# Optimization experiments

Measured on AMD Instinct MI355X. Metric: run time of the kernel, lower is better.

Reference implementation:

```python
import jax, jax.numpy as jnp
import numpy as np

EPS = 1e-12
K_APPNP = 3
ALPHA = 0.5

def setup_inputs() -> dict:
    key = jax.random.key(0)
    kg, kz, k1, k2, k3 = jax.random.split(key, 5)
    N, out_dim, hid_dim = 10000, 128, 256
    g = jax.random.uniform(kg, (N, N), dtype=jnp.float32)
    z = jax.random.normal(kz, (N, out_dim), dtype=jnp.float32)
    def xavier(k, shape):
        fan_out, fan_in = shape
        lim = float(np.sqrt(6.0 / (fan_in + fan_out)))
        return jax.random.uniform(k, shape, jnp.float32, -lim, lim)
    # torch Linear weight is [out_features, in_features]
    W1 = xavier(k1, (hid_dim, out_dim))    # res1: out_dim -> hid_dim
    W1_ = xavier(k2, (hid_dim, hid_dim))   # res1_: hid -> hid
    W2 = xavier(k3, (out_dim, hid_dim))    # res2: hid -> out_dim
    return {"g": g, "z": z, "W1": W1, "W1_": W1_, "W2": W2}

def _graph_conv(g, x, W, act):
    # dropout is identity in eval mode
    return act((g @ x) @ W.T)

def _appnp(g, H):
    Z = H
    for _ in range(K_APPNP):
        Z = (1.0 - ALPHA) * (g @ Z) + ALPHA * H
    return Z

def reference(g, z, W1, W1_, W2):
    z1 = _graph_conv(g, z, W1, jax.nn.relu)       # [N, hid]
    z_ = _graph_conv(g, z1, W1_, jax.nn.relu)     # [N, hid]
    # torch.tensor(z_) detaches from the autograd graph
    zn = jax.lax.stop_gradient(z_)
    norm = jnp.maximum(jnp.linalg.norm(zn, axis=1, keepdims=True), EPS)
    zn = zn / norm                                 # F.normalize(p=2, dim=1)
    Z = _appnp(g, zn)                              # [N, hid]
    res = _graph_conv(g, z_, W2, jax.nn.sigmoid)   # [N, out]
    return (res, Z)
```

## Files before the change

kernel.cpp:

```cpp
#include <hip/hip_runtime.h>
#include <stdint.h>

typedef __attribute__((ext_vector_type(8))) short short8;
typedef __attribute__((ext_vector_type(4))) float f32x4;
typedef __attribute__((ext_vector_type(4))) unsigned short us4;

#define MFMA16(a,b,c) __builtin_amdgcn_mfma_f32_16x16x32_bf16((a),(b),(c),0,0,0)

static __device__ __forceinline__ float bf2f(unsigned short u){
  union { float f; unsigned int i; } c; c.i = ((unsigned int)u) << 16; return c.f;
}
static __device__ __forceinline__ unsigned short f2bf(float f){
  union { float f; unsigned int i; } c; c.f = f;
  unsigned int x = c.i;
  unsigned int r = x + 0x7fffu + ((x >> 16) & 1u);
  return (unsigned short)(r >> 16);
}
static __device__ __forceinline__ short8 pack8(const float* v){
  short8 r;
  #pragma unroll
  for (int i = 0; i < 8; ++i) r[i] = (short)f2bf(v[i]);
  return r;
}

typedef const __attribute__((address_space(1))) void cg_void;
typedef __attribute__((address_space(3))) void lds_void;
static __device__ __forceinline__ void gl_lds16(const void* g, void* l){
  __builtin_amdgcn_global_load_lds((cg_void*)g, (lds_void*)l, 16, 0, 0);
}

#define MROWS 10240LL
#define LDA   10048

__global__ void k_zero(unsigned short* __restrict__ Tbuf){
  short8 z = {0,0,0,0,0,0,0,0};
  for (int c = blockIdx.x*256 + threadIdx.x; c < 512*6; c += gridDim.x*256){
    int row = c/6, k = c%6;
    *(short8*)(Tbuf + (long long)row*LDA + 10000 + k*8) = z;
  }
}

__global__ void k_conv_w(const float* __restrict__ a, unsigned short* __restrict__ oa, int na4,
                         const float* __restrict__ b, unsigned short* __restrict__ ob, int nb4,
                         const float* __restrict__ c, unsigned short* __restrict__ oc, int nc4){
  for (int i = blockIdx.x*blockDim.x + threadIdx.x; i < na4 + nb4 + nc4;
       i += gridDim.x*blockDim.x){
    const float* src; unsigned short* dst; int j = i;
    if (j < na4){ src = a; dst = oa; }
    else if (j < na4 + nb4){ j -= na4; src = b; dst = ob; }
    else { j -= na4 + nb4; src = c; dst = oc; }
    float4 f = *(const float4*)(src + (long long)j*4);
    us4 v; v.x=f2bf(f.x); v.y=f2bf(f.y); v.z=f2bf(f.z); v.w=f2bf(f.w);
    *(us4*)(dst + (long long)j*4) = v;
  }
}

__global__ void k_tconv_z(const float* __restrict__ z, unsigned short* __restrict__ o){
  __shared__ unsigned short t[64][65];
  const int rb = blockIdx.x*64, cb = blockIdx.y*64;
  #pragma unroll
  for (int it = 0; it < 4; ++it){
    int idx = it*256 + threadIdx.x;
    int r = idx >> 4, c4 = (idx & 15) * 4;
    float4 f = {0.f,0.f,0.f,0.f};
    if (rb + r < 10000) f = *(const float4*)(z + (long long)(rb+r)*128 + cb + c4);
    t[c4+0][r] = f2bf(f.x); t[c4+1][r] = f2bf(f.y);
    t[c4+2][r] = f2bf(f.z); t[c4+3][r] = f2bf(f.w);
  }
  __syncthreads();
  #pragma unroll
  for (int it = 0; it < 4; ++it){
    int idx = it*256 + threadIdx.x;
    int ro = idx >> 4, co4 = (idx & 15) * 4;
    us4 v; v.x=t[ro][co4]; v.y=t[ro][co4+1]; v.z=t[ro][co4+2]; v.w=t[ro][co4+3];
    *(us4*)(o + (long long)(cb+ro)*LDA + rb + co4) = v;
  }
}

__global__ __launch_bounds__(512)
void k_gemm_t0(const float* __restrict__ g, const unsigned short* __restrict__ zT,
               unsigned short* __restrict__ g16, unsigned short* __restrict__ P, int S)
{
  constexpr int ldp = 128;
  __shared__ unsigned short sm[2][24576];

  const int tid = threadIdx.x;
  const int wid = tid >> 6, l = tid & 63;
  const int wm = wid >> 1, wn = wid & 1;
  const int lr = l & 15, lk = l >> 4;
  const int mBase = blockIdx.x * 256;
  const int s = blockIdx.z;
  const int kt0 = (157*s)/S, kt1 = (157*(s+1))/S;

  int arow[4], acol8[4];
  #pragma unroll
  for (int i = 0; i < 4; ++i){
    int ch = tid + 512*i;
    int row = ch >> 3, gr = ch & 7;
    arow[i] = row; acol8[i] = ((gr ^ (row & 7)) * 8);
  }
  float fA[4][8];
  auto loadA = [&](int kt){
    #pragma unroll
    for (int i = 0; i < 4; ++i){
      int grow = mBase + arow[i];
      int col = kt*64 + acol8[i];
      if (grow < 10000 && col < 10000){
        float4 x = *(const float4*)(g + (long long)grow*10000 + col);
        float4 y = *(const float4*)(g + (long long)grow*10000 + col + 4);
        fA[i][0]=x.x; fA[i][1]=x.y; fA[i][2]=x.z; fA[i][3]=x.w;
        fA[i][4]=y.x; fA[i][5]=y.y; fA[i][6]=y.z; fA[i][7]=y.w;
      } else {
        #pragma unroll
        for (int j = 0; j < 8; ++j) fA[i][j] = 0.f;
      }
    }
  };
  auto writeA = [&](int buf, int kt){
    #pragma unroll
    for (int i = 0; i < 4; ++i){
      int ch = tid + 512*i;
      short8 v = pack8(fA[i]);
      *(short8*)(&sm[buf][ch*8]) = v;
      *(short8*)(g16 + (long long)(mBase + arow[i])*LDA + kt*64 + acol8[i]) = v;
    }
  };
  auto stageB = [&](int buf, int kt){
    unsigned short* dst = &sm[buf][16384];
    const unsigned short* Bk = zT + (long long)kt*64;
    #pragma unroll
    for (int i = 0; i < 2; ++i){
      int c = i*512 + tid; int row = c >> 3, gr = c & 7;
      gl_lds16(Bk + (long long)row*LDA + ((gr ^ (row & 7))*8), dst + c*8);
    }
  };

  f32x4 acc[4][4];
  #pragma unroll
  for (int i = 0; i < 4; ++i)
    #pragma unroll
    for (int j = 0; j < 4; ++j){ f32x4 zz = {0.f,0.f,0.f,0.f}; acc[i][j] = zz; }

  loadA(kt0); stageB(0, kt0); writeA(0, kt0);
  int cur = 0;
  for (int kt = kt0; kt < kt1; ++kt){
    __syncthreads();
    const bool pf = (kt + 1 < kt1);
    if (pf){ loadA(kt+1); stageB(cur^1, kt+1); }
    const unsigned short* sp = &sm[cur][0];
    #pragma unroll
    for (int ks = 0; ks < 2; ++ks){
      short8 a[4];
      #pragma unroll
      for (int i = 0; i < 4; ++i){
        int row = wm*64 + i*16 + lr;
        a[i] = *(const short8*)(sp + row*64 + (((4*ks+lk) ^ (row & 7))*8));
      }
      #pragma unroll
      for (int j = 0; j < 4; ++j){
        int rb = wn*64 + j*16 + lr;
        short8 b = *(const short8*)(sp + 16384 + rb*64 + (((4*ks+lk) ^ (rb & 7))*8));
        #pragma unroll
        for (int i = 0; i < 4; ++i)
          acc[i][j] = MFMA16(a[i], b, acc[i][j]);
      }
    }
    if (pf) writeA(cur^1, kt+1);
    cur ^= 1;
  }

  unsigned short* Pp = P + (long long)s*MROWS*ldp;
  #pragma unroll
  for (int i = 0; i < 4; ++i){
    const int row0 = mBase + wm*64 + i*16 + lk*4;
    #pragma unroll
    for (int j = 0; j < 4; ++j){
      const int col = wn*64 + j*16 + lr;
      #pragma unroll
      for (int r = 0; r < 4; ++r)
        Pp[(long long)(row0+r)*ldp + col] = f2bf(acc[i][j][r]);
    }
  }
}

template<int BN>
__global__ __launch_bounds__(512)
void k_gemm8(const unsigned short* __restrict__ A,
             const unsigned short* __restrict__ B,
             unsigned short* __restrict__ P, int S, int ldp, int nBase)
{
  constexpr int WNS = BN/4;
  constexpr int NJ  = WNS/16;
  constexpr int BCH = BN/64;
  constexpr int NLD = 4 + BCH;
  __shared__ unsigned short sm[2][16384 + BN*64];

  const int tid = threadIdx.x;
  const int wid = tid >> 6, l = tid & 63;
  const int wm = wid >> 2, wn = wid & 3;
  const int lr = l & 15, lk = l >> 4;
  const int mBase = blockIdx.x * 256;
  const int s = blockIdx.z;
  const int kt0 = (157*s)/S, kt1 = (157*(s+1))/S;

  const unsigned short* gsrc[NLD];
  int ldst[NLD];
  #pragma unroll
  for (int i = 0; i < 4; ++i){
    int ch = tid + 512*i;
    int row = ch >> 3, gc = (ch & 7) ^ (row & 7);
    gsrc[i] = A + (long long)(mBase + row)*LDA + gc*8;
    ldst[i] = ch*8;
  }
  #pragma unroll
  for (int i = 0; i < BCH; ++i){
    int ch = tid + 512*i;
    int row = ch >> 3, gc = (ch & 7) ^ (row & 7);
    gsrc[4+i] = B + (long long)(nBase + row)*LDA + gc*8;
    ldst[4+i] = 16384 + ch*8;
  }
  auto stage_tile = [&](unsigned short* dst, int kt){
    const long long ko = (long long)kt * 64;
    #pragma unroll
    for (int i = 0; i < NLD; ++i)
      gl_lds16(gsrc[i] + ko, dst + ldst[i]);
  };

  f32x4 acc[8][NJ];
  #pragma unroll
  for (int i = 0; i < 8; ++i)
    #pragma unroll
    for (int j = 0; j < NJ; ++j){ f32x4 zz = {0.f,0.f,0.f,0.f}; acc[i][j] = zz; }

  stage_tile(&sm[0][0], kt0);

  int cur = 0;
  for (int kt = kt0; kt < kt1; ++kt){
    const bool pf = (kt + 1 < kt1);
    unsigned short* nb = &sm[cur ^ 1][0];
    const unsigned short* sp = &sm[cur][0];

    if (pf){
      stage_tile(nb, kt + 1);
      __builtin_amdgcn_sched_barrier(0);
      if constexpr (BN == 256) asm volatile("s_waitcnt vmcnt(8)" ::: "memory");
      else                     asm volatile("s_waitcnt vmcnt(6)" ::: "memory");
    } else {
      asm volatile("s_waitcnt vmcnt(0)" ::: "memory");
    }
    __builtin_amdgcn_sched_barrier(0);
    __builtin_amdgcn_s_barrier();
    __builtin_amdgcn_sched_barrier(0);

    short8 bfr[NJ][2];
    #pragma unroll
    for (int jj = 0; jj < NJ; ++jj){
      const int row = wn*WNS + jj*16 + lr;
      #pragma unroll
      for (int ks = 0; ks < 2; ++ks)
        bfr[jj][ks] = *(const short8*)(sp + 16384 + row*64 + (((ks*4+lk) ^ (row & 7))*8));
    }
    #pragma unroll
    for (int ih = 0; ih < 2; ++ih){
      short8 af[4][2];
      #pragma unroll
      for (int ii = 0; ii < 4; ++ii){
        const int row = wm*128 + ih*64 + ii*16 + lr;
        #pragma unroll
        for (int ks = 0; ks < 2; ++ks)
          af[ii][ks] = *(const short8*)(sp + row*64 + (((ks*4+lk) ^ (row & 7))*8));
      }
      __builtin_amdgcn_s_setprio(1);
      #pragma unroll
      for (int ks = 0; ks < 2; ++ks)
        #pragma unroll
        for (int ii = 0; ii < 4; ++ii)
          #pragma unroll
          for (int jj = 0; jj < NJ; ++jj)
            acc[ih*4+ii][jj] = MFMA16(af[ii][ks], bfr[jj][ks], acc[ih*4+ii][jj]);
      __builtin_amdgcn_s_setprio(0);
    }
    __builtin_amdgcn_sched_barrier(0);
    __builtin_amdgcn_s_barrier();
    __builtin_amdgcn_sched_barrier(0);
    cur ^= 1;
  }

  unsigned short* Pp = P + (long long)s*MROWS*ldp;
  #pragma unroll
  for (int i = 0; i < 8; ++i){
    const int row0 = mBase + wm*128 + i*16 + lk*4;
    #pragma unroll
    for (int j = 0; j < NJ; ++j){
      const int col = nBase + wn*WNS + j*16 + lr;
      #pragma unroll
      for (int r = 0; r < 4; ++r)
        Pp[(long long)(row0+r)*ldp + col] = f2bf(acc[i][j][r]);
    }
  }
}

template<int NW, int KW, int LDP, int S, int MODE>
__global__ __launch_bounds__(320)
void k_small(const unsigned short* __restrict__ P,
             const unsigned short* __restrict__ W,
             unsigned short* __restrict__ o1,
             unsigned short* __restrict__ o2,
             unsigned short* __restrict__ o3,
             int doRelu)
{
  const int tid = threadIdx.x, w = tid >> 6, l = tid & 63;
  const int lr = l & 15, lk = l >> 4;
  const int mBase = blockIdx.x * 80;
  constexpr int NF = NW/16;
  constexpr long long SSTR = MROWS*(long long)LDP;

  f32x4 acc[NF];
  #pragma unroll
  for (int f = 0; f < NF; ++f){ f32x4 zz = {0.f,0.f,0.f,0.f}; acc[f] = zz; }

  const unsigned short* ap = P + (long long)(mBase + 16*w + lr)*LDP + lk*8;
  #pragma unroll
  for (int kc = 0; kc < KW/32; ++kc){
    float av[8];
    short8 v0 = *(const short8*)(ap + kc*32);
    #pragma unroll
    for (int e = 0; e < 8; ++e) av[e] = bf2f((unsigned short)v0[e]);
    #pragma unroll
    for (int s2 = 1; s2 < S; ++s2){
      short8 v = *(const short8*)(ap + (long long)s2*SSTR + kc*32);
      #pragma unroll
      for (int e = 0; e < 8; ++e) av[e] += bf2f((unsigned short)v[e]);
    }
    short8 a = pack8(av);
    #pragma unroll
    for (int f = 0; f < NF; ++f){
      short8 b = *(const short8*)(W + (long long)(16*f+lr)*KW + kc*32 + lk*8);
      acc[f] = MFMA16(a, b, acc[f]);
    }
  }

  const int row0 = mBase + 16*w + lk*4;
  if constexpr (MODE == 0){
    #pragma unroll
    for (int f = 0; f < NF; ++f){
      us4 v;
      #pragma unroll
      for (int r = 0; r < 4; ++r){
        float x = acc[f][r];
        if (doRelu) x = fmaxf(x, 0.0f);
        v[r] = f2bf(x);
      }
      *(us4*)(o1 + (long long)(16*f+lr)*LDA + row0) = v;
    }
  } else {
    float ss[4] = {0.f,0.f,0.f,0.f};
    #pragma unroll
    for (int f = 0; f < NF; ++f)
      #pragma unroll
      for (int r = 0; r < 4; ++r){
        float v = fmaxf(acc[f][r], 0.0f);
        acc[f][r] = v;
        ss[r] += v*v;
      }
    #pragma unroll
    for (int r = 0; r < 4; ++r){
      #pragma unroll
      for (int off = 1; off <= 8; off <<= 1)
        ss[r] += __shfl_xor(ss[r], off, 64);
      ss[r] = 1.0f / fmaxf(sqrtf(ss[r]), 1e-12f);
    }
    #pragma unroll
    for (int f = 0; f < NF; ++f){
      const int col = 16*f + lr;
      us4 vn;
      #pragma unroll
      for (int r = 0; r < 4; ++r){
        float zr = acc[f][r];
        float nr = zr * ss[r];
        vn[r] = f2bf(nr);
        o2[(long long)(row0+r)*256 + col] = vn[r];
        o3[(long long)(row0+r)*256 + col] = f2bf(zr);
      }
      *(us4*)(o1 + (long long)col*LDA + row0) = vn;
    }
  }
}

__global__ void k_reduce_T(const unsigned short* __restrict__ P, int S, int ldp, int colOff,
                           unsigned short* __restrict__ outT,
                           const unsigned short* __restrict__ H)
{
  __shared__ unsigned short t[64][65];
  const int rb = blockIdx.x*64, cb = blockIdx.y*64;
  const long long stride = MROWS * (long long)ldp;
  #pragma unroll
  for (int it = 0; it < 4; ++it){
    int idx = it*256 + threadIdx.x;
    int r = idx >> 4, c4 = (idx & 15)*4;
    int row = rb + r;
    float sv[4] = {0.f,0.f,0.f,0.f};
    if (row < 10000){
      const unsigned short* p = P + (long long)row*ldp + colOff + cb + c4;
      for (int s2 = 0; s2 < S; ++s2){
        us4 tt = *(const us4*)(p + (long long)s2*stride);
        sv[0] += bf2f(tt.x); sv[1] += bf2f(tt.y);
        sv[2] += bf2f(tt.z); sv[3] += bf2f(tt.w);
      }
      us4 h = *(const us4*)(H + (long long)row*256 + cb + c4);
      sv[0] = 0.5f*sv[0] + 0.5f*bf2f(h.x);
      sv[1] = 0.5f*sv[1] + 0.5f*bf2f(h.y);
      sv[2] = 0.5f*sv[2] + 0.5f*bf2f(h.z);
      sv[3] = 0.5f*sv[3] + 0.5f*bf2f(h.w);
    }
    t[c4+0][r] = f2bf(sv[0]); t[c4+1][r] = f2bf(sv[1]);
    t[c4+2][r] = f2bf(sv[2]); t[c4+3][r] = f2bf(sv[3]);
  }
  __syncthreads();
  #pragma unroll
  for (int it = 0; it < 4; ++it){
    int idx = it*256 + threadIdx.x;
    int ro = idx >> 4, co4 = (idx & 15)*4;
    us4 v; v.x=t[ro][co4]; v.y=t[ro][co4+1]; v.z=t[ro][co4+2]; v.w=t[ro][co4+3];
    *(us4*)(outT + (long long)(cb+ro)*LDA + rb + co4) = v;
  }
}

__global__ void k_reduce_sig(const unsigned short* __restrict__ P, int S,
                             float* __restrict__ out)
{
  const long long stride = MROWS * 128LL;
  const int idx = blockIdx.x*256 + threadIdx.x;
  const int row = idx >> 5;
  const int c4 = (idx & 31)*4;
  const unsigned short* p = P + (long long)row*128 + c4;
  float sv[4] = {0.f,0.f,0.f,0.f};
  for (int s2 = 0; s2 < S; ++s2){
    us4 tt = *(const us4*)(p + (long long)s2*stride);
    sv[0] += bf2f(tt.x); sv[1] += bf2f(tt.y);
    sv[2] += bf2f(tt.z); sv[3] += bf2f(tt.w);
  }
  float4 o;
  o.x = 1.0f/(1.0f + expf(-sv[0]));
  o.y = 1.0f/(1.0f + expf(-sv[1]));
  o.z = 1.0f/(1.0f + expf(-sv[2]));
  o.w = 1.0f/(1.0f + expf(-sv[3]));
  *(float4*)(out + (long long)row*128 + c4) = o;
}

__global__ void k_reduce2(const unsigned short* __restrict__ P, int S, int ldp,
                          float* __restrict__ out, const unsigned short* __restrict__ H)
{
  const long long stride = MROWS * (long long)ldp;
  const int idx = blockIdx.x*256 + threadIdx.x;
  const int row = idx >> 6;
  const int c4 = (idx & 63)*4;
  const unsigned short* p = P + (long long)row*ldp + c4;
  float sv[4] = {0.f,0.f,0.f,0.f};
  for (int s2 = 0; s2 < S; ++s2){
    us4 tt = *(const us4*)(p + (long long)s2*stride);
    sv[0] += bf2f(tt.x); sv[1] += bf2f(tt.y);
    sv[2] += bf2f(tt.z); sv[3] += bf2f(tt.w);
  }
  us4 h = *(const us4*)(H + (long long)row*256 + c4);
  float4 o;
  o.x = 0.5f*sv[0] + 0.5f*bf2f(h.x);
  o.y = 0.5f*sv[1] + 0.5f*bf2f(h.y);
  o.z = 0.5f*sv[2] + 0.5f*bf2f(h.z);
  o.w = 0.5f*sv[3] + 0.5f*bf2f(h.w);
  *(float4*)(out + (long long)row*256 + c4) = o;
}

extern "C" void kernel_launch(void* const* d_in, const int* in_sizes, int n_in,
                              void* d_out, int out_size, void* d_ws, size_t ws_size,
                              hipStream_t stream)
{
  const float* g   = (const float*)d_in[0];
  const float* z   = (const float*)d_in[1];
  const float* W1  = (const float*)d_in[2];
  const float* W1_ = (const float*)d_in[3];
  const float* W2  = (const float*)d_in[4];

  char* ws = (char*)d_ws;
  size_t off = 0;
  auto alloc = [&](size_t bytes)->void*{
    void* p = ws + off; off += (bytes + 255) & ~(size_t)255; return p;
  };
  unsigned short* g16  = (unsigned short*)alloc(10240ULL*10048*2);
  unsigned short* zT   = (unsigned short*)alloc(128ULL*10048*2);
  unsigned short* W1c  = (unsigned short*)alloc(256ULL*128*2);
  unsigned short* W1_c = (unsigned short*)alloc(256ULL*256*2);
  unsigned short* W2c  = (unsigned short*)alloc(128ULL*256*2);
  unsigned short* Tbuf = (unsigned short*)alloc(512ULL*10048*2);
  unsigned short* zn   = (unsigned short*)alloc(10000ULL*256*2);
  unsigned short* Xbuf = (unsigned short*)alloc(10000ULL*256*2);
  unsigned short* P    = (unsigned short*)alloc(10240ULL*1536*2);
  (void)ws_size; (void)in_sizes; (void)n_in; (void)out_size;

  float* res  = (float*)d_out;
  float* Zout = (float*)d_out + 10000LL*128;
  unsigned short* y2T = Tbuf + 256LL*LDA;

  k_zero<<<dim3(12), dim3(256), 0, stream>>>(Tbuf);
  k_tconv_z<<<dim3(157,2), dim3(256), 0, stream>>>(z, zT);
  k_conv_w<<<dim3(120), dim3(256), 0, stream>>>(W1, W1c, 256*128/4,
                                                W1_, W1_c, 256*256/4,
                                                W2, W2c, 128*256/4);

  k_gemm_t0<<<dim3(40,1,6), dim3(512), 0, stream>>>(g, zT, g16, P, 6);
  k_small<256,128,128,6,0><<<dim3(125), dim3(320), 0, stream>>>(P, W1c, Tbuf, nullptr, nullptr, 1);
  k_gemm8<256><<<dim3(40,1,6), dim3(512), 0, stream>>>(g16, Tbuf, P, 6, 256, 0);
  k_small<256,256,256,6,1><<<dim3(125), dim3(320), 0, stream>>>(P, W1_c, Tbuf, zn, Xbuf, 0);
  k_small<128,256,256,1,0><<<dim3(125), dim3(320), 0, stream>>>(Xbuf, W2c, y2T, nullptr, nullptr, 0);
  k_gemm8<256><<<dim3(40,1,6), dim3(512), 0, stream>>>(g16, Tbuf, P, 6, 256, 0);
  k_reduce_T<<<dim3(157,4), dim3(256), 0, stream>>>(P, 6, 256, 0, Tbuf, zn);
  k_gemm8<128><<<dim3(40,1,6), dim3(512), 0, stream>>>(g16, y2T, P, 6, 128, 0);
  k_reduce_sig<<<dim3(1250), dim3(256), 0, stream>>>(P, 6, res);
  k_gemm8<256><<<dim3(40,1,6), dim3(512), 0, stream>>>(g16, Tbuf, P, 6, 256, 0);
  k_reduce_T<<<dim3(157,4), dim3(256), 0, stream>>>(P, 6, 256, 0, Tbuf, zn);
  k_gemm8<256><<<dim3(40,1,6), dim3(512), 0, stream>>>(g16, Tbuf, P, 6, 256, 0);
  k_reduce2<<<dim3(2500), dim3(256), 0, stream>>>(P, 6, 256, Zout, zn);
}
```

Baseline: 551.0 us.

## Store bf16 graph in pre-swizzled contiguous tile-major layout

The first GEMM now writes the bf16 copy of g as contiguous 256x64 tiles, ordered by M-tile then K-tile, already in LDS swizzle order, instead of row-major with a padded stride. Later GEMMs stage A tiles with fully contiguous 16-byte global-to-LDS loads using a single base pointer. This is meant to improve DRAM and TLB locality for the repeated passes over g and to cut per-thread address registers. The layout is now tied to the 256x64 tile shape and the swizzle pattern, so any GEMM that reads g16 must use exactly that tiling.

```diff
diff --git a/kernel.cpp b/kernel.cpp
--- a/kernel.cpp
+++ b/kernel.cpp
@@ -31,6 +31,7 @@
 
 #define MROWS 10240LL
 #define LDA   10048
+#define GTILE 16384LL
 
 __global__ void k_zero(unsigned short* __restrict__ Tbuf){
   short8 z = {0,0,0,0,0,0,0,0};
@@ -88,7 +89,8 @@
   const int wid = tid >> 6, l = tid & 63;
   const int wm = wid >> 1, wn = wid & 1;
   const int lr = l & 15, lk = l >> 4;
-  const int mBase = blockIdx.x * 256;
+  const int mtile = blockIdx.x;
+  const int mBase = mtile * 256;
   const int s = blockIdx.z;
   const int kt0 = (157*s)/S, kt1 = (157*(s+1))/S;
 
@@ -117,12 +119,13 @@
     }
   };
   auto writeA = [&](int buf, int kt){
+    unsigned short* gt = g16 + ((long long)mtile*157 + kt)*GTILE;
     #pragma unroll
     for (int i = 0; i < 4; ++i){
       int ch = tid + 512*i;
       short8 v = pack8(fA[i]);
       *(short8*)(&sm[buf][ch*8]) = v;
-      *(short8*)(g16 + (long long)(mBase + arow[i])*LDA + kt*64 + acol8[i]) = v;
+      *(short8*)(gt + ch*8) = v;
     }
   };
   auto stageB = [&](int buf, int kt){
@@ -192,7 +195,6 @@
   constexpr int WNS = BN/4;
   constexpr int NJ  = WNS/16;
   constexpr int BCH = BN/64;
-  constexpr int NLD = 4 + BCH;
   __shared__ unsigned short sm[2][16384 + BN*64];
 
   const int tid = threadIdx.x;
@@ -203,27 +205,25 @@
   const int s = blockIdx.z;
   const int kt0 = (157*s)/S, kt1 = (157*(s+1))/S;
 
-  const unsigned short* gsrc[NLD];
-  int ldst[NLD];
-  #pragma unroll
-  for (int i = 0; i < 4; ++i){
-    int ch = tid + 512*i;
-    int row = ch >> 3, gc = (ch & 7) ^ (row & 7);
-    gsrc[i] = A + (long long)(mBase + row)*LDA + gc*8;
-    ldst[i] = ch*8;
-  }
+  const unsigned short* Abase = A + (long long)blockIdx.x*157*GTILE + tid*8;
+  const unsigned short* gsrcB[BCH];
+  int ldstB[BCH];
   #pragma unroll
   for (int i = 0; i < BCH; ++i){
     int ch = tid + 512*i;
     int row = ch >> 3, gc = (ch & 7) ^ (row & 7);
-    gsrc[4+i] = B + (long long)(nBase + row)*LDA + gc*8;
-    ldst[4+i] = 16384 + ch*8;
+    gsrcB[i] = B + (long long)(nBase + row)*LDA + gc*8;
+    ldstB[i] = 16384 + ch*8;
   }
   auto stage_tile = [&](unsigned short* dst, int kt){
+    const unsigned short* Ak = Abase + (long long)kt*GTILE;
+    #pragma unroll
+    for (int i = 0; i < 4; ++i)
+      gl_lds16(Ak + i*4096, dst + tid*8 + i*4096);
     const long long ko = (long long)kt * 64;
     #pragma unroll
-    for (int i = 0; i < NLD; ++i)
-      gl_lds16(gsrc[i] + ko, dst + ldst[i]);
+    for (int i = 0; i < BCH; ++i)
+      gl_lds16(gsrcB[i] + ko, dst + ldstB[i]);
   };
 
   f32x4 acc[8][NJ];
@@ -486,7 +486,7 @@
   auto alloc = [&](size_t bytes)->void*{
     void* p = ws + off; off += (bytes + 255) & ~(size_t)255; return p;
   };
-  unsigned short* g16  = (unsigned short*)alloc(10240ULL*10048*2);
+  unsigned short* g16  = (unsigned short*)alloc(40ULL*157*GTILE*2);
   unsigned short* zT   = (unsigned short*)alloc(128ULL*10048*2);
   unsigned short* W1c  = (unsigned short*)alloc(256ULL*128*2);
   unsigned short* W1_c = (unsigned short*)alloc(256ULL*256*2);
```

Measured after the change: 542.9 us. Within noise of the previous version (-1.5%).
